# Kernel optimization log

Hardware: AMD Instinct MI355X
Metric: run time of the kernel (lower is better)

## Reference

```python
import jax, jax.numpy as jnp
import numpy as np

EMBED = 1024
B, S = 4, 2048


def setup_inputs() -> dict:
    key = jax.random.key(0)
    ks = jax.random.split(key, 10)
    scale = 1.0 / np.sqrt(EMBED)
    return {
        "query": jax.random.normal(ks[0], (B, S, EMBED), jnp.float32),
        "key": jax.random.normal(ks[1], (B, S, EMBED), jnp.float32),
        "value": jax.random.normal(ks[2], (B, S, EMBED), jnp.float32),
        "attn_mask": jnp.zeros((B, S, S), jnp.float32),
        "Wq": jax.random.normal(ks[3], (EMBED, EMBED), jnp.float32) * scale,
        "bq": jnp.zeros((EMBED,), jnp.float32),
        "Wk": jax.random.normal(ks[4], (EMBED, EMBED), jnp.float32) * scale,
        "bk": jnp.zeros((EMBED,), jnp.float32),
        "Wv": jax.random.normal(ks[5], (EMBED, EMBED), jnp.float32) * scale,
        "bv": jnp.zeros((EMBED,), jnp.float32),
    }


def reference(query, key, value, attn_mask, Wq, bq, Wk, bk, Wv, bv):
    # Linear projections (torch Linear: x @ W.T + b)
    q = jnp.einsum("bse,fe->bsf", query, Wq) + bq
    k = jnp.einsum("bse,fe->bsf", key, Wk) + bk
    v = jnp.einsum("bse,fe->bsf", value, Wv) + bv
    # Scaled dot-product attention; NOTE: scale is sqrt(embed_size) (full dim),
    # matching the original module exactly (num_heads is unused there).
    inv_scale = 1.0 / jnp.sqrt(jnp.asarray(q.shape[-1], q.dtype))
    qk = jnp.einsum("bqe,bke->bqk", q, k) * inv_scale + attn_mask
    attn = jax.nn.softmax(qk, axis=-1)
    # dropout_p = 0.0 (eval-mode identity)
    return jnp.einsum("bqk,bke->bqe", attn, v)
```

## Files before the change

kernel.cpp:

```cpp
#include <hip/hip_runtime.h>
#include <stdint.h>


typedef __attribute__((ext_vector_type(8))) short s8v;
typedef __attribute__((ext_vector_type(4))) float f32x4;

__device__ __forceinline__ unsigned short f2b(float f) {
  union { float f; unsigned u; } c; c.f = f;
  unsigned r = c.u + 0x7fffu + ((c.u >> 16) & 1u);
  return (unsigned short)(r >> 16);
}

__device__ __forceinline__ void gload_lds16(const void* gsrc, void* ldst) {
  __builtin_amdgcn_global_load_lds(
      (__attribute__((address_space(1))) unsigned int*)(uintptr_t)gsrc,
      (__attribute__((address_space(3))) unsigned int*)(unsigned)(uintptr_t)ldst,
      16, 0, 0);
}

template <int N> __device__ __forceinline__ void waitvm() {
  if constexpr (N == 4)      asm volatile("s_waitcnt vmcnt(4)" ::: "memory");
  else if constexpr (N == 3) asm volatile("s_waitcnt vmcnt(3)" ::: "memory");
  else                       asm volatile("s_waitcnt vmcnt(0)" ::: "memory");
}

struct Job {
  const unsigned short* A; const unsigned short* B; void* C;
  const float* bias; const float* mask; float* sRow;
  long sAb, sBb, sCb, sMb;
  int lda, ldb, ldc, ldM;
  int K, tilesN, tilesMN;
  float scale; int bmode;
};

template <int NFRAG, int MODE>
__global__ __launch_bounds__(512, 2) void gemmJ(Job j0, Job j1, Job j2,
                                                int b0, int b1) {
  constexpr int BN = NFRAG * 64;
  constexpr int ASLOT = 256 * 64;
  constexpr int BSLOT = BN * 64;
  constexpr int SLOT = ASLOT + BSLOT;
  constexpr int CH = SLOT / 1024;
  constexpr int GPW = CH / 8;
  static_assert(4 * SLOT <= 160 * 1024, "LDS budget");
  __shared__ __align__(16) char lds[4 * SLOT];

  const int nwg = gridDim.x;
  const int hw = blockIdx.x;
  int g = (hw & 7) * (nwg >> 3) + (hw >> 3);
  const Job J = (g < b0) ? j0 : (g < b1) ? j1 : j2;
  g -= (g < b0) ? 0 : (g < b1) ? b0 : b1;

  const int batch = g / J.tilesMN;
  const int tt = g - batch * J.tilesMN;
  const int tm = tt / J.tilesN, tn = tt - tm * J.tilesN;
  const int brow = tm << 8, bcol = tn * BN;

  const int tid = threadIdx.x;
  const int lane = tid & 63, w = tid >> 6;
  const int wm = w >> 2, wn = w & 3;
  const int fr = lane & 15, fq = lane >> 4;

  const unsigned short* Ab = J.A + (long)batch * J.sAb;
  const unsigned short* Bb = J.B + (long)batch * J.sBb;

  const unsigned short* gsrc[GPW];
  int ldsdst[GPW];
#pragma unroll
  for (int i = 0; i < GPW; i++) {
    const int c = w + i * 8;
    const bool isA = (c < 16);
    const int cc = isA ? c : c - 16;
    const int roff = cc * 1024 + lane * 16;
    const int L = roff ^ (((roff >> 7) & 7) << 4);
    const int row = L >> 6, colb = L & 63;
    gsrc[i] = (isA ? (Ab + (long)(brow + row) * J.lda)
                   : (Bb + (long)(bcol + row) * J.ldb)) + (colb >> 1);
    ldsdst[i] = (isA ? 0 : ASLOT) + cc * 1024;
  }

  int offA[8], offB[NFRAG];
#pragma unroll
  for (int mi = 0; mi < 8; mi++) {
    const int oa = (wm * 128 + mi * 16 + fr) * 64 + fq * 16;
    offA[mi] = oa ^ (((oa >> 7) & 7) << 4);
  }
#pragma unroll
  for (int ni = 0; ni < NFRAG; ni++) {
    const int ob = (wn * (NFRAG * 16) + ni * 16 + fr) * 64 + fq * 16;
    offB[ni] = ASLOT + (ob ^ (((ob >> 7) & 7) << 4));
  }

  f32x4 acc[8][NFRAG];
#pragma unroll
  for (int mi = 0; mi < 8; mi++)
#pragma unroll
    for (int ni = 0; ni < NFRAG; ni++) acc[mi][ni] = (f32x4){0.f, 0.f, 0.f, 0.f};

  const int NT = J.K >> 5;

#define STAGE(kt) { \
  char* const sb_ = lds + ((kt) & 3) * SLOT; \
  _Pragma("unroll") \
  for (int i_ = 0; i_ < GPW; i_++) \
    gload_lds16(gsrc[i_] + (long)(kt) * 32, sb_ + ldsdst[i_]); }

  STAGE(0);
  STAGE(1);
  waitvm<GPW>();
  __builtin_amdgcn_s_barrier();

  for (int t = 0; t < NT; ++t) {
    const char* sb = lds + (t & 3) * SLOT;
    if (t + 2 < NT) STAGE(t + 2);

    s8v bf[NFRAG], af[4];
#pragma unroll
    for (int ni = 0; ni < NFRAG; ni++) bf[ni] = *(const s8v*)(sb + offB[ni]);
#pragma unroll
    for (int mi = 0; mi < 4; mi++) af[mi] = *(const s8v*)(sb + offA[mi]);
    __builtin_amdgcn_s_setprio(1);
#pragma unroll
    for (int mi = 0; mi < 4; mi++)
#pragma unroll
      for (int ni = 0; ni < NFRAG; ni++)
        acc[mi][ni] = __builtin_amdgcn_mfma_f32_16x16x32_bf16(
            af[mi], bf[ni], acc[mi][ni], 0, 0, 0);
    __builtin_amdgcn_s_setprio(0);
#pragma unroll
    for (int mi = 0; mi < 4; mi++) af[mi] = *(const s8v*)(sb + offA[4 + mi]);
    __builtin_amdgcn_s_setprio(1);
#pragma unroll
    for (int mi = 0; mi < 4; mi++)
#pragma unroll
      for (int ni = 0; ni < NFRAG; ni++)
        acc[4 + mi][ni] = __builtin_amdgcn_mfma_f32_16x16x32_bf16(
            af[mi], bf[ni], acc[4 + mi][ni], 0, 0, 0);
    __builtin_amdgcn_s_setprio(0);

    if (t + 1 < NT) {
      if (t + 2 < NT) waitvm<GPW>();
      else            waitvm<0>();
      __builtin_amdgcn_s_barrier();
    }
  }

  unsigned short* Cb = (unsigned short*)J.C;
  float* Cf = (float*)J.C;
  const long cB = (long)batch * J.sCb;
  const float* maskB = (MODE == 1) ? (J.mask + (long)batch * J.sMb) : nullptr;
  float* sB = (MODE != 0) ? (J.sRow + batch * 2048) : nullptr;

#pragma unroll
  for (int mi = 0; mi < 8; mi++) {
    const int rbase = brow + wm * 128 + mi * 16 + fq * 4;

    if constexpr (MODE == 0) {
#pragma unroll
      for (int ni = 0; ni < NFRAG; ni++) {
        const int col = bcol + wn * (NFRAG * 16) + ni * 16 + fr;
        const float bc = (J.bmode == 1) ? J.bias[col] : 0.f;
#pragma unroll
        for (int r = 0; r < 4; r++) {
          const int row = rbase + r;
          float v = acc[mi][ni][r] + ((J.bmode == 2) ? J.bias[row] : bc);
          Cb[cB + (long)row * J.ldc + col] = f2b(v);
        }
      }
    } else if constexpr (MODE == 1) {
      float rs[4] = {0.f, 0.f, 0.f, 0.f};
#pragma unroll
      for (int ni = 0; ni < NFRAG; ni++) {
        const int col = bcol + wn * (NFRAG * 16) + ni * 16 + fr;
#pragma unroll
        for (int r = 0; r < 4; r++) {
          const int row = rbase + r;
          float v = acc[mi][ni][r] * J.scale + maskB[(long)row * J.ldM + col];
          v = __expf(v);
          Cb[cB + (long)row * J.ldc + col] = f2b(v);
          rs[r] += v;
        }
      }
#pragma unroll
      for (int off = 1; off < 16; off <<= 1) {
#pragma unroll
        for (int r = 0; r < 4; r++) rs[r] += __shfl_xor(rs[r], off, 64);
      }
      if (fr == 0) {
#pragma unroll
        for (int r = 0; r < 4; r++) atomicAdd(&sB[rbase + r], rs[r]);
      }
    } else {
      float inv[4];
#pragma unroll
      for (int r = 0; r < 4; r++) inv[r] = 1.0f / sB[rbase + r];
#pragma unroll
      for (int ni = 0; ni < NFRAG; ni++) {
        const int col = bcol + wn * (NFRAG * 16) + ni * 16 + fr;
#pragma unroll
        for (int r = 0; r < 4; r++) {
          const int row = rbase + r;
          Cf[cB + (long)row * J.ldc + col] = acc[mi][ni][r] * inv[r];
        }
      }
    }
  }
#undef STAGE
}

__global__ __launch_bounds__(256) void cvt7(
    const float* s0, unsigned short* d0, const float* s1, unsigned short* d1,
    const float* s2, unsigned short* d2, const float* s3, unsigned short* d3,
    const float* s4, unsigned short* d4, const float* s5, unsigned short* d5,
    float* sz) {
  int bid = blockIdx.x;
  if (bid >= 2688) {
    for (int i = (bid - 2688) * 256 + threadIdx.x; i < 8192; i += 2048)
      sz[i] = 0.f;
    return;
  }
  const float* src; unsigned short* dst; long n8; int lb, nb;
  if (bid < 2304) {
    int r = bid / 768; lb = bid - r * 768; nb = 768; n8 = 1048576;
    src = r == 0 ? s0 : r == 1 ? s1 : s2;
    dst = r == 0 ? d0 : r == 1 ? d1 : d2;
  } else {
    int r = (bid - 2304) / 128; lb = (bid - 2304) - r * 128; nb = 128; n8 = 131072;
    src = r == 0 ? s3 : r == 1 ? s4 : s5;
    dst = r == 0 ? d3 : r == 1 ? d4 : d5;
  }
  const long stride = (long)nb * 256;
  for (long i = (long)lb * 256 + threadIdx.x; i < n8; i += stride) {
    const float* p = src + i * 8;
    f32x4 va = *(const f32x4*)p;
    f32x4 vb = *(const f32x4*)(p + 4);
    s8v o;
    o[0] = (short)f2b(va[0]); o[1] = (short)f2b(va[1]);
    o[2] = (short)f2b(va[2]); o[3] = (short)f2b(va[3]);
    o[4] = (short)f2b(vb[0]); o[5] = (short)f2b(vb[1]);
    o[6] = (short)f2b(vb[2]); o[7] = (short)f2b(vb[3]);
    *(s8v*)(dst + i * 8) = o;
  }
}

extern "C" void kernel_launch(void* const* d_in, const int* in_sizes, int n_in,
                              void* d_out, int out_size, void* d_ws, size_t ws_size,
                              hipStream_t stream) {
  const float* q    = (const float*)d_in[0];
  const float* k    = (const float*)d_in[1];
  const float* v    = (const float*)d_in[2];
  const float* mask = (const float*)d_in[3];
  const float* Wq   = (const float*)d_in[4];
  const float* bq   = (const float*)d_in[5];
  const float* Wk   = (const float*)d_in[6];
  const float* bk   = (const float*)d_in[7];
  const float* Wv   = (const float*)d_in[8];
  const float* bv   = (const float*)d_in[9];
  float* out = (float*)d_out;

  const size_t MB = 1ull << 20;
  if (ws_size < 134 * MB) return;
  char* ws = (char*)d_ws;
  unsigned short* qb  = (unsigned short*)(ws + 0 * MB);
  unsigned short* kb  = (unsigned short*)(ws + 16 * MB);
  unsigned short* vT  = (unsigned short*)(ws + 32 * MB);
  float*          sRw = (float*)(ws + 48 * MB);
  unsigned short* Sb  = (unsigned short*)(ws + 80 * MB);
  unsigned short* xq  = (unsigned short*)(ws + 80 * MB);
  unsigned short* xk  = (unsigned short*)(ws + 96 * MB);
  unsigned short* xv  = (unsigned short*)(ws + 112 * MB);
  unsigned short* Wqb = (unsigned short*)(ws + 128 * MB);
  unsigned short* Wkb = (unsigned short*)(ws + 130 * MB);
  unsigned short* Wvb = (unsigned short*)(ws + 132 * MB);

  cvt7<<<2696, 256, 0, stream>>>(q, xq, k, xk, v, xv, Wq, Wqb, Wk, Wkb, Wv, Wvb,
                                 sRw);

  Job jq = { xq, Wqb, (void*)qb, bq, nullptr, nullptr, 0, 0, 0, 0,
             1024, 1024, 1024, 0, 1024, 8, 256, 1.0f, 1 };
  Job jk = { xk, Wkb, (void*)kb, bk, nullptr, nullptr, 0, 0, 0, 0,
             1024, 1024, 1024, 0, 1024, 8, 256, 1.0f, 1 };
  Job jv = { Wvb, xv, (void*)vT, bv, nullptr, nullptr, 0, 2048L * 1024,
             1024L * 2048, 0, 1024, 1024, 2048, 0, 1024, 16, 64, 1.0f, 2 };
  gemmJ<2, 0><<<768, 512, 0, stream>>>(jq, jk, jv, 256, 512);

  Job js = { qb, kb, (void*)Sb, nullptr, mask, sRw,
             2048L * 1024, 2048L * 1024, 2048L * 2048, 2048L * 2048,
             1024, 1024, 2048, 2048, 1024, 8, 64, 0.03125f, 0 };
  gemmJ<4, 1><<<256, 512, 0, stream>>>(js, js, js, 256, 256);

  Job jp = { Sb, vT, (void*)out, nullptr, nullptr, sRw,
             2048L * 2048, 1024L * 2048, 2048L * 1024, 0,
             2048, 2048, 1024, 0, 2048, 8, 64, 1.0f, 0 };
  gemmJ<2, 2><<<256, 512, 0, stream>>>(jp, jp, jp, 256, 256);
}
```

Measured before the change: 225.6 us.

## Split-K the attention PV GEMM into two halves with a combine kernel

The final P·V GEMM is split along the key dimension into two jobs of 1024 each, launched as 512 blocks instead of 256, so more CUs are busy. Each half writes unnormalized fp32 partials, one straight into the output and one into a workspace buffer. A new combine kernel adds the two partials and applies the softmax row normalization. This buys better occupancy on the last GEMM at the cost of an extra 32MB partial write plus a read-modify-write pass over the output and one more launch.

```diff
diff --git a/kernel.cpp b/kernel.cpp
--- a/kernel.cpp
+++ b/kernel.cpp
@@ -149,7 +149,7 @@
   float* Cf = (float*)J.C;
   const long cB = (long)batch * J.sCb;
   const float* maskB = (MODE == 1) ? (J.mask + (long)batch * J.sMb) : nullptr;
-  float* sB = (MODE != 0) ? (J.sRow + batch * 2048) : nullptr;
+  float* sB = (MODE == 1) ? (J.sRow + batch * 2048) : nullptr;
 
 #pragma unroll
   for (int mi = 0; mi < 8; mi++) {
@@ -191,21 +191,33 @@
         for (int r = 0; r < 4; r++) atomicAdd(&sB[rbase + r], rs[r]);
       }
     } else {
-      float inv[4];
-#pragma unroll
-      for (int r = 0; r < 4; r++) inv[r] = 1.0f / sB[rbase + r];
 #pragma unroll
       for (int ni = 0; ni < NFRAG; ni++) {
         const int col = bcol + wn * (NFRAG * 16) + ni * 16 + fr;
 #pragma unroll
         for (int r = 0; r < 4; r++) {
           const int row = rbase + r;
-          Cf[cB + (long)row * J.ldc + col] = acc[mi][ni][r] * inv[r];
+          Cf[cB + (long)row * J.ldc + col] = acc[mi][ni][r];
         }
       }
     }
   }
 #undef STAGE
+}
+
+__global__ __launch_bounds__(256) void combine(float* out, const float* P1,
+                                               const float* sR) {
+  const long n4 = 2097152;
+  const long stride = (long)gridDim.x * 256;
+  for (long j = (long)blockIdx.x * 256 + threadIdx.x; j < n4; j += stride) {
+    f32x4 a = ((const f32x4*)out)[j];
+    f32x4 b = ((const f32x4*)P1)[j];
+    const float inv = 1.0f / sR[j >> 8];
+    f32x4 r;
+    r[0] = (a[0] + b[0]) * inv; r[1] = (a[1] + b[1]) * inv;
+    r[2] = (a[2] + b[2]) * inv; r[3] = (a[3] + b[3]) * inv;
+    ((f32x4*)out)[j] = r;
+  }
 }
 
 __global__ __launch_bounds__(256) void cvt7(
@@ -265,6 +277,7 @@
   unsigned short* kb  = (unsigned short*)(ws + 16 * MB);
   unsigned short* vT  = (unsigned short*)(ws + 32 * MB);
   float*          sRw = (float*)(ws + 48 * MB);
+  float*          P1  = (float*)(ws + 64 * MB);
   unsigned short* Sb  = (unsigned short*)(ws + 80 * MB);
   unsigned short* xq  = (unsigned short*)(ws + 80 * MB);
   unsigned short* xk  = (unsigned short*)(ws + 96 * MB);
@@ -289,8 +302,13 @@
              1024, 1024, 2048, 2048, 1024, 8, 64, 0.03125f, 0 };
   gemmJ<4, 1><<<256, 512, 0, stream>>>(js, js, js, 256, 256);
 
-  Job jp = { Sb, vT, (void*)out, nullptr, nullptr, sRw,
+  Job p0 = { Sb, vT, (void*)out, nullptr, nullptr, nullptr,
              2048L * 2048, 1024L * 2048, 2048L * 1024, 0,
-             2048, 2048, 1024, 0, 2048, 8, 64, 1.0f, 0 };
-  gemmJ<2, 2><<<256, 512, 0, stream>>>(jp, jp, jp, 256, 256);
-}
+             2048, 2048, 1024, 0, 1024, 8, 64, 1.0f, 0 };
+  Job p1 = { Sb + 1024, vT + 1024, (void*)P1, nullptr, nullptr, nullptr,
+             2048L * 2048, 1024L * 2048, 2048L * 1024, 0,
+             2048, 2048, 1024, 0, 1024, 8, 64, 1.0f, 0 };
+  gemmJ<2, 2><<<512, 512, 0, stream>>>(p0, p1, p1, 256, 512);
+
+  combine<<<2048, 256, 0, stream>>>(out, P1, sRw);
+}
```

After: 249.9 us. 1.11x slower.

## Fuse fp32-to-bf16 conversion into QKV projection GEMM loads

Applied to the files above, without the earlier changes.

Removes the separate conversion kernel that wrote bf16 copies of the activations and weights. A new projection GEMM loads fp32 directly into registers, packs it to bf16 with v_cvt_pk_bf16_f32, and writes swizzled tiles to LDS behind a register double-buffered pipeline. This saves a full extra read and write pass over about 100MB of inputs. In exchange the GEMM reads twice the bytes per tile and loses the asynchronous global-to-LDS loads, which may expose latency. The weights are also re-converted by every tile that uses them.

```diff
diff --git a/kernel.cpp b/kernel.cpp
--- a/kernel.cpp
+++ b/kernel.cpp
@@ -4,6 +4,7 @@
 
 typedef __attribute__((ext_vector_type(8))) short s8v;
 typedef __attribute__((ext_vector_type(4))) float f32x4;
+typedef __attribute__((ext_vector_type(4))) unsigned u32x4;
 
 __device__ __forceinline__ unsigned short f2b(float f) {
   union { float f; unsigned u; } c; c.f = f;
@@ -22,6 +23,157 @@
   if constexpr (N == 4)      asm volatile("s_waitcnt vmcnt(4)" ::: "memory");
   else if constexpr (N == 3) asm volatile("s_waitcnt vmcnt(3)" ::: "memory");
   else                       asm volatile("s_waitcnt vmcnt(0)" ::: "memory");
+}
+
+struct JobF {
+  const float* A; const float* B; unsigned short* C; const float* bias;
+  long sAb, sBb, sCb;
+  int lda, ldb, ldc, tilesN, tilesMN, bmode;
+};
+
+__global__ __launch_bounds__(512, 2) void gemmF(JobF j0, JobF j1, JobF j2,
+                                                int b0, int b1) {
+  constexpr int ASLOT = 256 * 64;
+  constexpr int SLOT = ASLOT + 128 * 64;
+  constexpr int NT = 32;
+  __shared__ __align__(16) char lds[4 * SLOT];
+
+  const int nwg = gridDim.x;
+  const int hw = blockIdx.x;
+  int g = (hw & 7) * (nwg >> 3) + (hw >> 3);
+  const JobF J = (g < b0) ? j0 : (g < b1) ? j1 : j2;
+  g -= (g < b0) ? 0 : (g < b1) ? b0 : b1;
+
+  const int batch = g / J.tilesMN;
+  const int tt = g - batch * J.tilesMN;
+  const int tm = tt / J.tilesN, tn = tt - tm * J.tilesN;
+  const int brow = tm << 8, bcol = tn << 7;
+
+  const int tid = threadIdx.x, lane = tid & 63, w = tid >> 6;
+  const int wm = w >> 2, wn = w & 3;
+  const int fr = lane & 15, fq = lane >> 4;
+
+  const float* Ab = J.A + (long)batch * J.sAb;
+  const float* Bb = J.B + (long)batch * J.sBb;
+
+  const float* gsrcF[3];
+  int ldsdst[3];
+#pragma unroll
+  for (int i = 0; i < 3; i++) {
+    const int c = w + i * 8;
+    const bool isA = (c < 16);
+    const int cc = isA ? c : c - 16;
+    const int roff = cc * 1024 + lane * 16;
+    const int L = roff ^ (((roff >> 7) & 7) << 4);
+    const int row = L >> 6, elem = (L & 63) >> 1;
+    gsrcF[i] = (isA ? (Ab + (long)(brow + row) * J.lda)
+                    : (Bb + (long)(bcol + row) * J.ldb)) + elem;
+    ldsdst[i] = (isA ? 0 : ASLOT) + cc * 1024 + lane * 16;
+  }
+
+  int offA[8], offB[2];
+#pragma unroll
+  for (int mi = 0; mi < 8; mi++) {
+    const int oa = (wm * 128 + mi * 16 + fr) * 64 + fq * 16;
+    offA[mi] = oa ^ (((oa >> 7) & 7) << 4);
+  }
+#pragma unroll
+  for (int ni = 0; ni < 2; ni++) {
+    const int ob = (wn * 32 + ni * 16 + fr) * 64 + fq * 16;
+    offB[ni] = ASLOT + (ob ^ (((ob >> 7) & 7) << 4));
+  }
+
+  f32x4 acc[8][2];
+#pragma unroll
+  for (int mi = 0; mi < 8; mi++)
+#pragma unroll
+    for (int ni = 0; ni < 2; ni++) acc[mi][ni] = (f32x4){0.f, 0.f, 0.f, 0.f};
+
+  f32x4 eLo[3], eHi[3], oLo[3], oHi[3];
+
+#define ISSUE(kt, LO, HI) { \
+  _Pragma("unroll") \
+  for (int i_ = 0; i_ < 3; i_++) { \
+    const float* p_ = gsrcF[i_] + (long)(kt) * 32; \
+    LO[i_] = *(const f32x4*)p_; HI[i_] = *(const f32x4*)(p_ + 4); } }
+
+#define CVTWRITE(kt, LO, HI) { \
+  char* const sb_ = lds + ((kt) & 3) * SLOT; \
+  _Pragma("unroll") \
+  for (int i_ = 0; i_ < 3; i_++) { \
+    unsigned o0_, o1_, o2_, o3_; \
+    asm("v_cvt_pk_bf16_f32 %0, %1, %2" : "=v"(o0_) : "v"(LO[i_][0]), "v"(LO[i_][1])); \
+    asm("v_cvt_pk_bf16_f32 %0, %1, %2" : "=v"(o1_) : "v"(LO[i_][2]), "v"(LO[i_][3])); \
+    asm("v_cvt_pk_bf16_f32 %0, %1, %2" : "=v"(o2_) : "v"(HI[i_][0]), "v"(HI[i_][1])); \
+    asm("v_cvt_pk_bf16_f32 %0, %1, %2" : "=v"(o3_) : "v"(HI[i_][2]), "v"(HI[i_][3])); \
+    *(u32x4*)(sb_ + ldsdst[i_]) = (u32x4){o0_, o1_, o2_, o3_}; } }
+
+#define MFMA_BODY(t) { \
+  const char* sb_ = lds + ((t) & 3) * SLOT; \
+  s8v bf_[2], af_[4]; \
+  _Pragma("unroll") \
+  for (int ni_ = 0; ni_ < 2; ni_++) bf_[ni_] = *(const s8v*)(sb_ + offB[ni_]); \
+  _Pragma("unroll") \
+  for (int mi_ = 0; mi_ < 4; mi_++) af_[mi_] = *(const s8v*)(sb_ + offA[mi_]); \
+  __builtin_amdgcn_s_setprio(1); \
+  _Pragma("unroll") \
+  for (int mi_ = 0; mi_ < 4; mi_++) \
+    _Pragma("unroll") \
+    for (int ni_ = 0; ni_ < 2; ni_++) \
+      acc[mi_][ni_] = __builtin_amdgcn_mfma_f32_16x16x32_bf16( \
+          af_[mi_], bf_[ni_], acc[mi_][ni_], 0, 0, 0); \
+  __builtin_amdgcn_s_setprio(0); \
+  _Pragma("unroll") \
+  for (int mi_ = 0; mi_ < 4; mi_++) af_[mi_] = *(const s8v*)(sb_ + offA[4 + mi_]); \
+  __builtin_amdgcn_s_setprio(1); \
+  _Pragma("unroll") \
+  for (int mi_ = 0; mi_ < 4; mi_++) \
+    _Pragma("unroll") \
+    for (int ni_ = 0; ni_ < 2; ni_++) \
+      acc[4 + mi_][ni_] = __builtin_amdgcn_mfma_f32_16x16x32_bf16( \
+          af_[mi_], bf_[ni_], acc[4 + mi_][ni_], 0, 0, 0); \
+  __builtin_amdgcn_s_setprio(0); }
+
+#define GATE(kt, LO, HI) { \
+  CVTWRITE(kt, LO, HI); \
+  asm volatile("s_waitcnt lgkmcnt(0)" ::: "memory"); \
+  __builtin_amdgcn_s_barrier(); }
+
+  ISSUE(0, eLo, eHi);
+  ISSUE(1, oLo, oHi);
+  GATE(0, eLo, eHi);
+
+  for (int t = 0; t < NT; t += 2) {
+    if (t + 2 < NT) ISSUE(t + 2, eLo, eHi);
+    MFMA_BODY(t);
+    if (t + 1 < NT) GATE(t + 1, oLo, oHi);
+    if (t + 1 < NT) {
+      if (t + 3 < NT) ISSUE(t + 3, oLo, oHi);
+      MFMA_BODY(t + 1);
+      if (t + 2 < NT) GATE(t + 2, eLo, eHi);
+    }
+  }
+
+  const long cB = (long)batch * J.sCb;
+#pragma unroll
+  for (int mi = 0; mi < 8; mi++) {
+    const int rbase = brow + wm * 128 + mi * 16 + fq * 4;
+#pragma unroll
+    for (int ni = 0; ni < 2; ni++) {
+      const int col = bcol + wn * 32 + ni * 16 + fr;
+      const float bc = (J.bmode == 1) ? J.bias[col] : 0.f;
+#pragma unroll
+      for (int r = 0; r < 4; r++) {
+        const int row = rbase + r;
+        float v = acc[mi][ni][r] + ((J.bmode == 2) ? J.bias[row] : bc);
+        J.C[cB + (long)row * J.ldc + col] = f2b(v);
+      }
+    }
+  }
+#undef ISSUE
+#undef CVTWRITE
+#undef MFMA_BODY
+#undef GATE
 }
 
 struct Job {
@@ -149,25 +301,13 @@
   float* Cf = (float*)J.C;
   const long cB = (long)batch * J.sCb;
   const float* maskB = (MODE == 1) ? (J.mask + (long)batch * J.sMb) : nullptr;
-  float* sB = (MODE != 0) ? (J.sRow + batch * 2048) : nullptr;
+  float* sB = (J.sRow != nullptr) ? (J.sRow + batch * 2048) : nullptr;
 
 #pragma unroll
   for (int mi = 0; mi < 8; mi++) {
     const int rbase = brow + wm * 128 + mi * 16 + fq * 4;
 
-    if constexpr (MODE == 0) {
-#pragma unroll
-      for (int ni = 0; ni < NFRAG; ni++) {
-        const int col = bcol + wn * (NFRAG * 16) + ni * 16 + fr;
-        const float bc = (J.bmode == 1) ? J.bias[col] : 0.f;
-#pragma unroll
-        for (int r = 0; r < 4; r++) {
-          const int row = rbase + r;
-          float v = acc[mi][ni][r] + ((J.bmode == 2) ? J.bias[row] : bc);
-          Cb[cB + (long)row * J.ldc + col] = f2b(v);
-        }
-      }
-    } else if constexpr (MODE == 1) {
+    if constexpr (MODE == 1) {
       float rs[4] = {0.f, 0.f, 0.f, 0.f};
 #pragma unroll
       for (int ni = 0; ni < NFRAG; ni++) {
@@ -208,39 +348,8 @@
 #undef STAGE
 }
 
-__global__ __launch_bounds__(256) void cvt7(
-    const float* s0, unsigned short* d0, const float* s1, unsigned short* d1,
-    const float* s2, unsigned short* d2, const float* s3, unsigned short* d3,
-    const float* s4, unsigned short* d4, const float* s5, unsigned short* d5,
-    float* sz) {
-  int bid = blockIdx.x;
-  if (bid >= 2688) {
-    for (int i = (bid - 2688) * 256 + threadIdx.x; i < 8192; i += 2048)
-      sz[i] = 0.f;
-    return;
-  }
-  const float* src; unsigned short* dst; long n8; int lb, nb;
-  if (bid < 2304) {
-    int r = bid / 768; lb = bid - r * 768; nb = 768; n8 = 1048576;
-    src = r == 0 ? s0 : r == 1 ? s1 : s2;
-    dst = r == 0 ? d0 : r == 1 ? d1 : d2;
-  } else {
-    int r = (bid - 2304) / 128; lb = (bid - 2304) - r * 128; nb = 128; n8 = 131072;
-    src = r == 0 ? s3 : r == 1 ? s4 : s5;
-    dst = r == 0 ? d3 : r == 1 ? d4 : d5;
-  }
-  const long stride = (long)nb * 256;
-  for (long i = (long)lb * 256 + threadIdx.x; i < n8; i += stride) {
-    const float* p = src + i * 8;
-    f32x4 va = *(const f32x4*)p;
-    f32x4 vb = *(const f32x4*)(p + 4);
-    s8v o;
-    o[0] = (short)f2b(va[0]); o[1] = (short)f2b(va[1]);
-    o[2] = (short)f2b(va[2]); o[3] = (short)f2b(va[3]);
-    o[4] = (short)f2b(vb[0]); o[5] = (short)f2b(vb[1]);
-    o[6] = (short)f2b(vb[2]); o[7] = (short)f2b(vb[3]);
-    *(s8v*)(dst + i * 8) = o;
-  }
+__global__ __launch_bounds__(256) void zeroS(float* sz) {
+  sz[blockIdx.x * 256 + threadIdx.x] = 0.f;
 }
 
 extern "C" void kernel_launch(void* const* d_in, const int* in_sizes, int n_in,
@@ -266,23 +375,14 @@
   unsigned short* vT  = (unsigned short*)(ws + 32 * MB);
   float*          sRw = (float*)(ws + 48 * MB);
   unsigned short* Sb  = (unsigned short*)(ws + 80 * MB);
-  unsigned short* xq  = (unsigned short*)(ws + 80 * MB);
-  unsigned short* xk  = (unsigned short*)(ws + 96 * MB);
-  unsigned short* xv  = (unsigned short*)(ws + 112 * MB);
-  unsigned short* Wqb = (unsigned short*)(ws + 128 * MB);
-  unsigned short* Wkb = (unsigned short*)(ws + 130 * MB);
-  unsigned short* Wvb = (unsigned short*)(ws + 132 * MB);
-
-  cvt7<<<2696, 256, 0, stream>>>(q, xq, k, xk, v, xv, Wq, Wqb, Wk, Wkb, Wv, Wvb,
-                                 sRw);
-
-  Job jq = { xq, Wqb, (void*)qb, bq, nullptr, nullptr, 0, 0, 0, 0,
-             1024, 1024, 1024, 0, 1024, 8, 256, 1.0f, 1 };
-  Job jk = { xk, Wkb, (void*)kb, bk, nullptr, nullptr, 0, 0, 0, 0,
-             1024, 1024, 1024, 0, 1024, 8, 256, 1.0f, 1 };
-  Job jv = { Wvb, xv, (void*)vT, bv, nullptr, nullptr, 0, 2048L * 1024,
-             1024L * 2048, 0, 1024, 1024, 2048, 0, 1024, 16, 64, 1.0f, 2 };
-  gemmJ<2, 0><<<768, 512, 0, stream>>>(jq, jk, jv, 256, 512);
+
+  zeroS<<<32, 256, 0, stream>>>(sRw);
+
+  JobF fq = { q, Wq, qb, bq, 0, 0, 0, 1024, 1024, 1024, 8, 256, 1 };
+  JobF fk = { k, Wk, kb, bk, 0, 0, 0, 1024, 1024, 1024, 8, 256, 1 };
+  JobF fv = { Wv, v, vT, bv, 0, 2048L * 1024, 1024L * 2048,
+              1024, 1024, 2048, 16, 64, 2 };
+  gemmF<<<768, 512, 0, stream>>>(fq, fk, fv, 256, 512);
 
   Job js = { qb, kb, (void*)Sb, nullptr, mask, sRw,
              2048L * 1024, 2048L * 1024, 2048L * 2048, 2048L * 2048,
```

After: 231.9 us. +2.8%, slower.
